# Kernel optimization log

Hardware: AMD Instinct MI355X
Metric: run time of the kernel (lower is better)

## Reference

```python
import jax, jax.numpy as jnp
from jax import lax
import numpy as np

DN = ('NCHW', 'OIHW', 'NCHW')

def conv2d(x, w, b, pad):
    y = lax.conv_general_dilated(x, w, (1, 1), [(pad, pad), (pad, pad)], dimension_numbers=DN)
    return y + b[None, :, None, None]

def setup_inputs() -> dict:
    key = jax.random.key(0)
    ks = jax.random.split(key, 20)
    B, C, H, W = 2, 256, 64, 64
    d = {}
    d['Fl'] = jax.random.normal(ks[0], (B, C, H, W), dtype=jnp.float32)
    d['Fv'] = jax.random.normal(ks[1], (B, C, H, W), dtype=jnp.float32)
    s3 = 1.0 / np.sqrt(C * 9)
    s1 = 1.0 / np.sqrt(C)
    names3 = ['Wqs', 'Wks', 'Wvs', 'Wqc', 'Wkc', 'Wvc']
    for i, n in enumerate(names3):
        d[n] = jax.random.normal(ks[2 + 2 * i], (C, C, 3, 3), dtype=jnp.float32) * s3
        d['b' + n[1:]] = jax.random.normal(ks[3 + 2 * i], (C,), dtype=jnp.float32) * 0.01
    d['Wgs'] = jax.random.normal(ks[14], (C, C, 1, 1), dtype=jnp.float32) * s1
    d['bgs'] = jax.random.normal(ks[15], (C,), dtype=jnp.float32) * 0.01
    d['Wfuse'] = jax.random.normal(ks[16], (C, 2 * C, 1, 1), dtype=jnp.float32) * (1.0 / np.sqrt(2 * C))
    d['bfuse'] = jax.random.normal(ks[17], (C,), dtype=jnp.float32) * 0.01
    return d

def reference(Fl, Fv, Wqs, bqs, Wks, bks, Wvs, bvs, Wqc, bqc, Wkc, bkc, Wvc, bvc, Wgs, bgs, Wfuse, bfuse):
    b, c, h, w = Fl.shape
    hw = h * w
    # --- self branch (on Fl) ---
    Qs = conv2d(Fl, Wqs, bqs, 1).reshape(b, c, hw)
    Ks = conv2d(Fl, Wks, bks, 1).reshape(b, c, hw)
    Vs = conv2d(Fl, Wvs, bvs, 1).reshape(b, c, hw)
    multi_s = jnp.einsum('bjk,bjq->bkq', Qs, Ks)          # [b, hw, hw]
    multi_s = jax.nn.softmax(multi_s, axis=1)              # softmax over dim=1 (as in torch code)
    Gs = jnp.einsum('bik,bjk->bij', multi_s, Vs)           # [b, hw, c]
    Gs = Gs.reshape(b, c, h, w)                            # raw reshape, faithful to torch
    Gs = conv2d(Gs, Wgs, bgs, 0) + Fl
    # --- cross branch (Q from Fl, K/V from Fv) ---
    Qc = conv2d(Fl, Wqc, bqc, 1).reshape(b, c, hw)
    Kc = conv2d(Fv, Wkc, bkc, 1).reshape(b, c, hw)
    Vc = conv2d(Fv, Wvc, bvc, 1).reshape(b, c, hw)
    multi_c = jnp.einsum('bjk,bjq->bkq', Qc, Kc)
    multi_c = jax.nn.softmax(multi_c, axis=1)
    Gc = jnp.einsum('bik,bjk->bij', multi_c, Vc)
    Gc = Gc.reshape(b, c, h, w)
    Gc = conv2d(Gc, Wgs, bgs, 0) + Fv                      # note: original uses Gs_conv for both branches
    out = conv2d(jnp.concatenate([Gs, Gc], axis=1), Wfuse, bfuse, 0)
    return out
```

## Files before the change

### kernel.cpp

```cpp
#include <hip/hip_runtime.h>

typedef __bf16 bf16x4 __attribute__((ext_vector_type(4)));
typedef __bf16 bf16x8 __attribute__((ext_vector_type(8)));
typedef float  f32x4  __attribute__((ext_vector_type(4)));

#define HWSZ 4096
#define CCH  256
#define LOG2E 1.44269504088896340736f

__device__ __forceinline__ float exp2_fast(float x) {
#if __has_builtin(__builtin_amdgcn_exp2f)
  return __builtin_amdgcn_exp2f(x);
#else
  return exp2f(x);
#endif
}

__device__ __forceinline__ void stage16(const __bf16* g, __bf16* ldsBase) {
#if __has_builtin(__builtin_amdgcn_global_load_lds)
  __builtin_amdgcn_global_load_lds(
      (const __attribute__((address_space(1))) void*)g,
      (__attribute__((address_space(3))) void*)ldsBase, 16, 0, 0);
#else
  int lane = threadIdx.x & 63;
  *(bf16x8*)(ldsBase + lane * 8) = *(const bf16x8*)g;
#endif
}

#define SWZ_STAGE(lane) ((((lane) & 3) ^ (((lane) >> 3) & 3)) * 8)
#define SWZ_READ(quad, lane) ((((quad) ^ (((lane) >> 1) & 3))) * 8)

__global__ __launch_bounds__(256)
void gemm_conv(const __bf16* __restrict__ AL, const __bf16* __restrict__ AV,
               const __bf16* __restrict__ Cc,
               __bf16* __restrict__ qst, __bf16* __restrict__ kst,
               __bf16* __restrict__ vs,  __bf16* __restrict__ qct,
               __bf16* __restrict__ kct, __bf16* __restrict__ vc,
               const float* __restrict__ bqs, const float* __restrict__ bks,
               const float* __restrict__ bvs, const float* __restrict__ bqc,
               const float* __restrict__ bkc, const float* __restrict__ bvc)
{
  __shared__ __align__(16) __bf16 smem[8192];
  __bf16* As = smem;
  __bf16* Bs = smem + 4096;

  const int tid  = threadIdx.x;
  const int lane = tid & 63;
  const int w    = tid >> 6;
  const int wm   = (w >> 1) * 64;
  const int wn   = (w & 1) * 64;
  const int z    = blockIdx.z;
  const int by   = blockIdx.y;
  const int bn   = blockIdx.x * 128;
  const int K    = 2304;

  const bool isL = (by < 8);
  const int bm = (isL ? by : by - 8) * 128;
  const __bf16* Ab = isL ? AL : AV;
  const __bf16* Bb = Cc + (long)((isL ? 0 : 2) + z) * 9437184;

  f32x4 acc[4][4] = {};
  const int srow = lane >> 2;
  const int skc  = SWZ_STAGE(lane);
  const int quad = lane >> 4, l15 = lane & 15;
  const int rdo  = SWZ_READ(quad, lane);

  for (int k0 = 0; k0 < K; k0 += 32) {
#pragma unroll
    for (int j = 0; j < 2; ++j) {
      int rbase = w * 32 + j * 16;
      stage16(Ab + (long)(bm + rbase + srow) * K + k0 + skc, As + rbase * 32);
    }
#pragma unroll
    for (int j = 0; j < 2; ++j) {
      int rbase = w * 32 + j * 16;
      stage16(Bb + (long)(bn + rbase + srow) * K + k0 + skc, Bs + rbase * 32);
    }
    __syncthreads();
    bf16x8 af[4], bfr[4];
#pragma unroll
    for (int t = 0; t < 4; ++t)
      af[t] = *(const bf16x8*)(As + (wm + t * 16 + l15) * 32 + rdo);
#pragma unroll
    for (int t = 0; t < 4; ++t)
      bfr[t] = *(const bf16x8*)(Bs + (wn + t * 16 + l15) * 32 + rdo);
#pragma unroll
    for (int mt = 0; mt < 4; ++mt)
#pragma unroll
      for (int nt = 0; nt < 4; ++nt)
        acc[mt][nt] = __builtin_amdgcn_mfma_f32_16x16x32_bf16(af[mt], bfr[nt], acc[mt][nt], 0, 0, 0);
    __syncthreads();
  }

#pragma unroll
  for (int mt = 0; mt < 4; ++mt) {
#pragma unroll
    for (int nt = 0; nt < 4; ++nt) {
#pragma unroll
      for (int r = 0; r < 4; ++r) {
        int m = bm + wm + mt * 16 + quad * 4 + r;
        int n = bn + wn + nt * 16 + l15;
        int g = m >> 8, mm = m & 255;
        const float* bias; __bf16* op; bool vlay;
        if (isL) {
          bias = (g == 0) ? bqs : (g == 1) ? bks : (g == 2) ? bvs : bqc;
          op   = (g == 0) ? qst : (g == 1) ? kst : (g == 2) ? vs  : qct;
          vlay = (g == 2);
        } else {
          bias = g ? bvc : bkc;
          op   = g ? vc  : kct;
          vlay = (g == 1);
        }
        float vv = acc[mt][nt][r] + bias[mm];
        if (vlay) op[(long)z * 1048576 + (long)mm * HWSZ + n] = (__bf16)vv;
        else      op[(long)z * 1048576 + (long)n * CCH + mm] = (__bf16)vv;
      }
    }
  }
}

__global__ __launch_bounds__(256)
void qk_stats(const __bf16* __restrict__ qs, const __bf16* __restrict__ qc,
              const __bf16* __restrict__ ks, const __bf16* __restrict__ kc,
              float* __restrict__ pm, float* __restrict__ pl)
{
  __shared__ __align__(16) __bf16 Kres[64 * 260];
  __shared__ float wm_[4][64], wl_[4][64];

  const int tid = threadIdx.x, lane = tid & 63, w = tid >> 6;
  const int quad = lane >> 4, l15 = lane & 15;
  const int lid = blockIdx.x;
  const int g = lid & 3;
  const int z = g & 1, br = g >> 1;
  const int ih = (lid >> 2) & 1;
  const int qb = (lid >> 3) * 64;
  const __bf16* Qt = (br ? qc : qs) + (long)z * 1048576;
  const __bf16* Kt = (br ? kc : ks) + (long)z * 1048576;

  for (int idx = tid; idx < 2048; idx += 256) {
    int r = idx >> 5, c8 = (idx & 31) * 8;
    *(bf16x8*)(Kres + r * 260 + c8) = *(const bf16x8*)(Kt + (long)(qb + r) * 256 + c8);
  }
  __syncthreads();

  float rm[4], rl[4];
#pragma unroll
  for (int nt = 0; nt < 4; ++nt) { rm[nt] = -3.0e38f; rl[nt] = 0.f; }

  for (int it = 0; it < 8; ++it) {
    const int i0 = ih * 2048 + it * 256 + w * 64;
    f32x4 accS[4][4] = {};
#pragma unroll
    for (int cs = 0; cs < 256; cs += 32) {
      bf16x8 a[4], b[4];
#pragma unroll
      for (int mt = 0; mt < 4; ++mt)
        a[mt] = *(const bf16x8*)(Qt + (long)(i0 + mt * 16 + l15) * 256 + cs + quad * 8);
#pragma unroll
      for (int nt = 0; nt < 4; ++nt)
        b[nt] = *(const bf16x8*)(Kres + (nt * 16 + l15) * 260 + cs + quad * 8);
#pragma unroll
      for (int mt = 0; mt < 4; ++mt)
#pragma unroll
        for (int nt = 0; nt < 4; ++nt)
          accS[mt][nt] = __builtin_amdgcn_mfma_f32_16x16x32_bf16(a[mt], b[nt], accS[mt][nt], 0, 0, 0);
    }
#pragma unroll
    for (int nt = 0; nt < 4; ++nt) {
      float mx = -3.0e38f;
#pragma unroll
      for (int mt = 0; mt < 4; ++mt)
#pragma unroll
        for (int r = 0; r < 4; ++r) mx = fmaxf(mx, accS[mt][nt][r]);
      float sl = 0.f;
#pragma unroll
      for (int mt = 0; mt < 4; ++mt)
#pragma unroll
        for (int r = 0; r < 4; ++r) sl += exp2_fast((accS[mt][nt][r] - mx) * LOG2E);
#pragma unroll
      for (int d = 16; d <= 32; d <<= 1) {
        float om = __shfl_xor(mx, d, 64);
        float ol = __shfl_xor(sl, d, 64);
        float nm = fmaxf(mx, om);
        sl = sl * exp2_fast((mx - nm) * LOG2E) + ol * exp2_fast((om - nm) * LOG2E);
        mx = nm;
      }
      float nm = fmaxf(rm[nt], mx);
      rl[nt] = rl[nt] * exp2_fast((rm[nt] - nm) * LOG2E) + sl * exp2_fast((mx - nm) * LOG2E);
      rm[nt] = nm;
    }
  }
  if (lane < 16) {
#pragma unroll
    for (int nt = 0; nt < 4; ++nt) { wm_[w][nt * 16 + lane] = rm[nt]; wl_[w][nt * 16 + lane] = rl[nt]; }
  }
  __syncthreads();
  if (tid < 64) {
    float m = -3.0e38f;
#pragma unroll
    for (int ww = 0; ww < 4; ++ww) m = fmaxf(m, wm_[ww][tid]);
    float l = 0.f;
#pragma unroll
    for (int ww = 0; ww < 4; ++ww)
      l += wl_[ww][tid] * exp2_fast((wm_[ww][tid] - m) * LOG2E);
    long o = ((long)ih * 4 + br * 2 + z) * 4096 + qb + tid;
    pm[o] = m;
    pl[o] = l;
  }
}

__global__ void stats_combine2(const float* __restrict__ pm, const float* __restrict__ pl,
                               float* __restrict__ mst, float* __restrict__ lst) {
  int q = blockIdx.x * 256 + threadIdx.x;
  int zbr = blockIdx.y;
  float m0 = pm[(long)zbr * 4096 + q],        l0 = pl[(long)zbr * 4096 + q];
  float m1 = pm[(long)(4 + zbr) * 4096 + q],  l1 = pl[(long)(4 + zbr) * 4096 + q];
  float m = fmaxf(m0, m1);
  float l = l0 * exp2_fast((m0 - m) * LOG2E) + l1 * exp2_fast((m1 - m) * LOG2E);
  mst[(long)zbr * 4096 + q] = m;
  lst[(long)zbr * 4096 + q] = 1.0f / l;
}

__global__ __launch_bounds__(256)
void fused_pv(const __bf16* __restrict__ qs, const __bf16* __restrict__ qc,
              const __bf16* __restrict__ ks, const __bf16* __restrict__ kc,
              const __bf16* __restrict__ vs, const __bf16* __restrict__ vc,
              const float* __restrict__ mst, const float* __restrict__ lst,
              float* __restrict__ gacc)
{
  __shared__ __align__(16) __bf16 Qres[64 * 260];
  __shared__ __align__(16) __bf16 Pl[64 * 132];
  __shared__ __align__(16) __bf16 Kst[128 * 32];

  const int tid = threadIdx.x, lane = tid & 63, w = tid >> 6;
  const int quad = lane >> 4, l15 = lane & 15;
  const int lid = blockIdx.x;
  const int g   = lid & 7;
  const int zbr = g >> 1;
  const int qh  = g & 1;
  const int bi  = (lid >> 3) * 64;
  const int br = zbr >> 1, z = zbr & 1;
  const __bf16* Qt = (br ? qc : qs) + (long)z * 1048576;
  const __bf16* Kt = (br ? kc : ks) + (long)z * 1048576;
  const __bf16* Vv = (br ? vc : vs) + (long)z * 1048576;
  const float* msp = mst + (long)zbr * 4096;
  const float* lsp = lst + (long)zbr * 4096;
  float* go = gacc + ((long)qh * 4 + zbr) * 1048576;

  for (int idx = tid; idx < 2048; idx += 256) {
    int r = idx >> 5, c8 = (idx & 31) * 8;
    *(bf16x8*)(Qres + r * 260 + c8) = *(const bf16x8*)(Qt + (long)(bi + r) * 256 + c8);
  }

  f32x4 accO[4][4] = {};
  const int srow = lane >> 2;
  const int skc  = SWZ_STAGE(lane);
  const int rdo  = SWZ_READ(quad, lane);
  const int q0 = qh * 2048;

  for (int qc0 = q0; qc0 < q0 + 2048; qc0 += 128) {
    f32x4 accS[4][2] = {};
#pragma unroll
    for (int cs = 0; cs < 256; cs += 32) {
#pragma unroll
      for (int jj = 0; jj < 2; ++jj) {
        int rbase = w * 32 + jj * 16;
        stage16(Kt + (long)(qc0 + rbase + srow) * 256 + cs + skc, Kst + rbase * 32);
      }
      __syncthreads();
      bf16x8 aq[4], bk[2];
#pragma unroll
      for (int mt = 0; mt < 4; ++mt)
        aq[mt] = *(const bf16x8*)(Qres + (mt * 16 + l15) * 260 + cs + quad * 8);
#pragma unroll
      for (int nt = 0; nt < 2; ++nt)
        bk[nt] = *(const bf16x8*)(Kst + (w * 32 + nt * 16 + l15) * 32 + rdo);
#pragma unroll
      for (int mt = 0; mt < 4; ++mt)
#pragma unroll
        for (int nt = 0; nt < 2; ++nt)
          accS[mt][nt] = __builtin_amdgcn_mfma_f32_16x16x32_bf16(aq[mt], bk[nt], accS[mt][nt], 0, 0, 0);
      __syncthreads();
    }
#pragma unroll
    for (int nt = 0; nt < 2; ++nt) {
      int q = w * 32 + nt * 16 + l15;
      float mq = msp[qc0 + q], lq = lsp[qc0 + q];
#pragma unroll
      for (int mt = 0; mt < 4; ++mt)
#pragma unroll
        for (int r = 0; r < 4; ++r) {
          int i = mt * 16 + quad * 4 + r;
          Pl[i * 132 + q] = (__bf16)(exp2_fast((accS[mt][nt][r] - mq) * LOG2E) * lq);
        }
    }
    __syncthreads();
#pragma unroll
    for (int qs0 = 0; qs0 < 128; qs0 += 32) {
      bf16x8 ap[4], bv[4];
#pragma unroll
      for (int mt = 0; mt < 4; ++mt)
        ap[mt] = *(const bf16x8*)(Pl + (mt * 16 + l15) * 132 + qs0 + quad * 8);
#pragma unroll
      for (int nt = 0; nt < 4; ++nt)
        bv[nt] = *(const bf16x8*)(Vv + (long)(w * 64 + nt * 16 + l15) * 4096 + qc0 + qs0 + quad * 8);
#pragma unroll
      for (int mt = 0; mt < 4; ++mt)
#pragma unroll
        for (int nt = 0; nt < 4; ++nt)
          accO[mt][nt] = __builtin_amdgcn_mfma_f32_16x16x32_bf16(ap[mt], bv[nt], accO[mt][nt], 0, 0, 0);
    }
  }
#pragma unroll
  for (int mt = 0; mt < 4; ++mt)
#pragma unroll
    for (int nt = 0; nt < 4; ++nt)
#pragma unroll
      for (int r = 0; r < 4; ++r) {
        int i = mt * 16 + quad * 4 + r;
        int j = w * 64 + nt * 16 + l15;
        go[(long)(bi + i) * 256 + j] = accO[mt][nt][r];
      }
}

__global__ __launch_bounds__(256)
void gsum_reshape(const float* __restrict__ ga, __bf16* __restrict__ gt) {
  __shared__ __bf16 lds[64 * 260];
  const int t = threadIdx.x, lane = t & 63, w = t >> 6;
  const int zbr = blockIdx.z;
  const int v   = blockIdx.y;
  const int jg  = blockIdx.x;
  const float* g0 = ga + (long)zbr * 1048576;
  const float* g1 = g0 + 4194304;
  for (int ci0 = 0; ci0 < 256; ci0 += 4) {
    int ci = ci0 + w;
    long src = (long)(ci * 16 + v) * 256 + jg * 64 + lane;
    lds[lane * 260 + ci] = (__bf16)(g0[src] + g1[src]);
  }
  __syncthreads();
  __bf16* out = gt + (long)zbr * 1048576 + ((long)v * 256 + jg * 64) * 256;
#pragma unroll
  for (int pp = 0; pp < 8; ++pp) {
    int idx = pp * 256 + t;
    int row = idx >> 5, c8 = (idx & 31) * 8;
    *(bf16x8*)(out + (long)row * 256 + c8) = *(const bf16x8*)(lds + row * 260 + c8);
  }
}

__global__ __launch_bounds__(256)
void wcomb(const float* __restrict__ Wgs, const float* __restrict__ bgs,
           const float* __restrict__ Wfu, const float* __restrict__ bfu,
           __bf16* __restrict__ WT, float* __restrict__ biasT)
{
  const int co = blockIdx.x, t = threadIdx.x;
  const float* wrow = Wfu + (long)co * 512;
  float accs = 0.f, accc = 0.f;
  for (int c = 0; c < 256; ++c) {
    float gv = Wgs[(long)c * 256 + t];
    accs = fmaf(wrow[c], gv, accs);
    accc = fmaf(wrow[c + 256], gv, accc);
  }
  __bf16* o = WT + (long)co * 1024;
  o[t]       = (__bf16)accs;
  o[256 + t] = (__bf16)accc;
  o[512 + t] = (__bf16)wrow[t];
  o[768 + t] = (__bf16)wrow[256 + t];
  __shared__ float red[256];
  red[t] = (wrow[t] + wrow[t + 256]) * bgs[t];
  __syncthreads();
  for (int s = 128; s > 0; s >>= 1) {
    if (t < s) red[t] += red[t + s];
    __syncthreads();
  }
  if (t == 0) biasT[co] = bfu[co] + red[0];
}

__global__ __launch_bounds__(256)
void tail_gemm(const __bf16* __restrict__ WT, const __bf16* __restrict__ GTS,
               const __bf16* __restrict__ Xt, const float* __restrict__ biasT,
               float* __restrict__ out)
{
  __shared__ __align__(16) __bf16 smem[8192];
  __bf16* As = smem;
  __bf16* Bs = smem + 4096;

  const int tid  = threadIdx.x;
  const int lane = tid & 63;
  const int w    = tid >> 6;
  const int wm   = (w >> 1) * 64;
  const int wn   = (w & 1) * 64;
  const int z    = blockIdx.z;
  const int bm   = blockIdx.y * 128;
  const int bn   = blockIdx.x * 128;

  const __bf16* Bsel[4] = {
    GTS + (long)z * 1048576, GTS + (long)(2 + z) * 1048576,
    Xt  + (long)z * 1048576, Xt  + (long)(2 + z) * 1048576
  };

  f32x4 acc[4][4] = {};
  const int srow = lane >> 2;
  const int skc  = SWZ_STAGE(lane);
  const int quad = lane >> 4, l15 = lane & 15;
  const int rdo  = SWZ_READ(quad, lane);

  for (int k0 = 0; k0 < 1024; k0 += 32) {
    const __bf16* Bb = Bsel[k0 >> 8];
    const int kk = k0 & 255;
#pragma unroll
    for (int j = 0; j < 2; ++j) {
      int rbase = w * 32 + j * 16;
      stage16(WT + (long)(bm + rbase + srow) * 1024 + k0 + skc, As + rbase * 32);
    }
#pragma unroll
    for (int j = 0; j < 2; ++j) {
      int rbase = w * 32 + j * 16;
      stage16(Bb + (long)(bn + rbase + srow) * 256 + kk + skc, Bs + rbase * 32);
    }
    __syncthreads();
    bf16x8 af[4], bfr[4];
#pragma unroll
    for (int t = 0; t < 4; ++t)
      af[t] = *(const bf16x8*)(As + (wm + t * 16 + l15) * 32 + rdo);
#pragma unroll
    for (int t = 0; t < 4; ++t)
      bfr[t] = *(const bf16x8*)(Bs + (wn + t * 16 + l15) * 32 + rdo);
#pragma unroll
    for (int mt = 0; mt < 4; ++mt)
#pragma unroll
      for (int nt = 0; nt < 4; ++nt)
        acc[mt][nt] = __builtin_amdgcn_mfma_f32_16x16x32_bf16(af[mt], bfr[nt], acc[mt][nt], 0, 0, 0);
    __syncthreads();
  }

#pragma unroll
  for (int mt = 0; mt < 4; ++mt)
#pragma unroll
    for (int nt = 0; nt < 4; ++nt)
#pragma unroll
      for (int r = 0; r < 4; ++r) {
        int m = bm + wm + mt * 16 + quad * 4 + r;
        int n = bn + wn + nt * 16 + l15;
        out[((long)z * 256 + m) * HWSZ + n] = acc[mt][nt][r] + biasT[m];
      }
}

__global__ void transpose_cvt(const float* __restrict__ F0, const float* __restrict__ F1,
                              __bf16* __restrict__ Xt) {
  __shared__ float tile[32][33];
  int img = blockIdx.z;
  const float* src = (img < 2 ? F0 : F1) + (long)(img & 1) * (CCH * HWSZ);
  __bf16* dst = Xt + (long)img * (HWSZ * CCH);
  int p0 = blockIdx.x * 32, c0 = blockIdx.y * 32;
  int tx = threadIdx.x, ty = threadIdx.y;
#pragma unroll
  for (int j = 0; j < 32; j += 8)
    tile[ty + j][tx] = src[(long)(c0 + ty + j) * HWSZ + p0 + tx];
  __syncthreads();
#pragma unroll
  for (int j = 0; j < 32; j += 8)
    dst[(long)(p0 + ty + j) * CCH + c0 + tx] = (__bf16)tile[tx][ty + j];
}

__global__ void im2col_k(const __bf16* __restrict__ Xt, __bf16* __restrict__ Cc) {
  int img = blockIdx.y;
  int e = blockIdx.x * 256 + threadIdx.x;
  int p = e / 288;
  int c8 = e - p * 288;
  int t = c8 >> 5;
  int ci0 = (c8 & 31) * 8;
  int dy = t / 3 - 1, dx = t - (t / 3) * 3 - 1;
  int y = p >> 6, x = p & 63;
  int yy = y + dy, xx = x + dx;
  const __bf16* src = Xt + (long)img * (HWSZ * CCH);
  __bf16* dst = Cc + (long)img * 9437184 + (long)p * 2304 + t * 256 + ci0;
  uint4 v = make_uint4(0u, 0u, 0u, 0u);
  if ((unsigned)yy < 64u && (unsigned)xx < 64u)
    v = *(const uint4*)(src + (long)(yy * 64 + xx) * CCH + ci0);
  *(uint4*)dst = v;
}

struct W6 { const float* w[6]; };
__global__ void repack_w3(W6 wp, __bf16* __restrict__ AL, __bf16* __restrict__ AV) {
  int zi = blockIdx.y;
  int e = blockIdx.x * 256 + threadIdx.x;
  int co = e / 2304;
  int rem = e - co * 2304;
  int t = rem >> 8, ci = rem & 255;
  float v = wp.w[zi][(long)co * 2304 + ci * 9 + t];
  __bf16* dst = (zi < 4) ? (AL + (long)zi * 256 * 2304) : (AV + (long)(zi - 4) * 256 * 2304);
  dst[(long)co * 2304 + rem] = (__bf16)v;
}

extern "C" void kernel_launch(void* const* d_in, const int* in_sizes, int n_in,
                              void* d_out, int out_size, void* d_ws, size_t ws_size,
                              hipStream_t stream) {
  const float* Fl  = (const float*)d_in[0];
  const float* Fv  = (const float*)d_in[1];
  const float* Wqs = (const float*)d_in[2];  const float* bqs = (const float*)d_in[3];
  const float* Wks = (const float*)d_in[4];  const float* bks = (const float*)d_in[5];
  const float* Wvs = (const float*)d_in[6];  const float* bvs = (const float*)d_in[7];
  const float* Wqc = (const float*)d_in[8];  const float* bqc = (const float*)d_in[9];
  const float* Wkc = (const float*)d_in[10]; const float* bkc = (const float*)d_in[11];
  const float* Wvc = (const float*)d_in[12]; const float* bvc = (const float*)d_in[13];
  const float* Wgs = (const float*)d_in[14]; const float* bgs = (const float*)d_in[15];
  const float* Wfu = (const float*)d_in[16]; const float* bfu = (const float*)d_in[17];

  char* ws = (char*)d_ws;
  size_t off = 0;
  auto take = [&](size_t bytes) -> void* {
    void* p = ws + off; off = (off + bytes + 255) & ~(size_t)255; return p;
  };
  __bf16* QST  = (__bf16*)take(4194304);
  __bf16* KST  = (__bf16*)take(4194304);
  __bf16* QCT  = (__bf16*)take(4194304);
  __bf16* KCT  = (__bf16*)take(4194304);
  __bf16* VS   = (__bf16*)take(4194304);
  __bf16* VC   = (__bf16*)take(4194304);
  __bf16* GTS  = (__bf16*)take(8388608);
  __bf16* AL   = (__bf16*)take(4718592);
  __bf16* AV   = (__bf16*)take(2359296);
  __bf16* WT   = (__bf16*)take(524288);
  float*  BT   = (float*)take(1024);
  float*  MST  = (float*)take(65536);
  float*  LST  = (float*)take(65536);
  float*  PM   = (float*)take(131072);
  float*  PL   = (float*)take(131072);
  __bf16* Xt   = (__bf16*)take(8388608);
  size_t ovl = off;
  __bf16* Cc = (__bf16*)take(75497472);
  size_t needConv = off;
  float* GACC = (float*)(ws + ovl);
  size_t needAttn = ovl + 33554432;
  size_t need = needConv > needAttn ? needConv : needAttn;
  if (ws_size < need) return;

  transpose_cvt<<<dim3(128, 8, 4), dim3(32, 8), 0, stream>>>(Fl, Fv, Xt);
  im2col_k<<<dim3(4608, 4), 256, 0, stream>>>(Xt, Cc);
  W6 wp; wp.w[0]=Wqs; wp.w[1]=Wks; wp.w[2]=Wvs; wp.w[3]=Wqc; wp.w[4]=Wkc; wp.w[5]=Wvc;
  repack_w3<<<dim3(2304, 6), 256, 0, stream>>>(wp, AL, AV);
  wcomb<<<dim3(256), 256, 0, stream>>>(Wgs, bgs, Wfu, bfu, WT, BT);

  gemm_conv<<<dim3(32, 12, 2), 256, 0, stream>>>(
      AL, AV, Cc, QST, KST, VS, QCT, KCT, VC,
      bqs, bks, bvs, bqc, bkc, bvc);

  qk_stats<<<dim3(512), 256, 0, stream>>>(QST, QCT, KST, KCT, PM, PL);
  stats_combine2<<<dim3(16, 4), 256, 0, stream>>>(PM, PL, MST, LST);

  fused_pv<<<dim3(512), 256, 0, stream>>>(
      QST, QCT, KST, KCT, VS, VC, MST, LST, GACC);

  gsum_reshape<<<dim3(4, 16, 4), 256, 0, stream>>>(GACC, GTS);

  tail_gemm<<<dim3(32, 2, 2), 256, 0, stream>>>(WT, GTS, Xt, BT, (float*)d_out);
}
```

Before: 442.9 us.

## Use 8 waves per block in fused_pv and read K directly from global

Doubles fused_pv's block size to 512 threads, so each wave computes a 16-column slice of the score tile and a 32-channel slice of the output, halving per-wave accumulator registers. The LDS staging of K tiles via global_load_lds, and its two barriers per k-step, is dropped; each wave now loads its K fragment straight from global memory. The aim is higher occupancy and fewer barriers, at the cost of uncoalesced, uncached-in-LDS K reads and more waves contending on the same Qres/Pl tiles.

```diff
diff --git a/kernel.cpp b/kernel.cpp
--- a/kernel.cpp
+++ b/kernel.cpp
@@ -221,7 +221,7 @@
   lst[(long)zbr * 4096 + q] = 1.0f / l;
 }
 
-__global__ __launch_bounds__(256)
+__global__ __launch_bounds__(512, 4)
 void fused_pv(const __bf16* __restrict__ qs, const __bf16* __restrict__ qc,
               const __bf16* __restrict__ ks, const __bf16* __restrict__ kc,
               const __bf16* __restrict__ vs, const __bf16* __restrict__ vc,
@@ -230,7 +230,6 @@
 {
   __shared__ __align__(16) __bf16 Qres[64 * 260];
   __shared__ __align__(16) __bf16 Pl[64 * 132];
-  __shared__ __align__(16) __bf16 Kst[128 * 32];
 
   const int tid = threadIdx.x, lane = tid & 63, w = tid >> 6;
   const int quad = lane >> 4, l15 = lane & 15;
@@ -247,78 +246,67 @@
   const float* lsp = lst + (long)zbr * 4096;
   float* go = gacc + ((long)qh * 4 + zbr) * 1048576;
 
-  for (int idx = tid; idx < 2048; idx += 256) {
+  for (int idx = tid; idx < 2048; idx += 512) {
     int r = idx >> 5, c8 = (idx & 31) * 8;
     *(bf16x8*)(Qres + r * 260 + c8) = *(const bf16x8*)(Qt + (long)(bi + r) * 256 + c8);
   }
-
-  f32x4 accO[4][4] = {};
-  const int srow = lane >> 2;
-  const int skc  = SWZ_STAGE(lane);
-  const int rdo  = SWZ_READ(quad, lane);
+  __syncthreads();
+
+  f32x4 accO[4][2] = {};
   const int q0 = qh * 2048;
+  const __bf16* Vl0 = Vv + (long)(w * 32 + l15) * 4096 + quad * 8;
+  const __bf16* Vl1 = Vl0 + (long)16 * 4096;
 
   for (int qc0 = q0; qc0 < q0 + 2048; qc0 += 128) {
-    f32x4 accS[4][2] = {};
+    f32x4 accS[4] = {};
+    const __bf16* Kl = Kt + (long)(qc0 + w * 16 + l15) * 256 + quad * 8;
 #pragma unroll
     for (int cs = 0; cs < 256; cs += 32) {
-#pragma unroll
-      for (int jj = 0; jj < 2; ++jj) {
-        int rbase = w * 32 + jj * 16;
-        stage16(Kt + (long)(qc0 + rbase + srow) * 256 + cs + skc, Kst + rbase * 32);
-      }
-      __syncthreads();
-      bf16x8 aq[4], bk[2];
+      bf16x8 aq[4];
+      bf16x8 bk = *(const bf16x8*)(Kl + cs);
 #pragma unroll
       for (int mt = 0; mt < 4; ++mt)
         aq[mt] = *(const bf16x8*)(Qres + (mt * 16 + l15) * 260 + cs + quad * 8);
 #pragma unroll
-      for (int nt = 0; nt < 2; ++nt)
-        bk[nt] = *(const bf16x8*)(Kst + (w * 32 + nt * 16 + l15) * 32 + rdo);
-#pragma unroll
-      for (int mt = 0; mt < 4; ++mt)
-#pragma unroll
-        for (int nt = 0; nt < 2; ++nt)
-          accS[mt][nt] = __builtin_amdgcn_mfma_f32_16x16x32_bf16(aq[mt], bk[nt], accS[mt][nt], 0, 0, 0);
-      __syncthreads();
-    }
-#pragma unroll
-    for (int nt = 0; nt < 2; ++nt) {
-      int q = w * 32 + nt * 16 + l15;
+      for (int mt = 0; mt < 4; ++mt)
+        accS[mt] = __builtin_amdgcn_mfma_f32_16x16x32_bf16(aq[mt], bk, accS[mt], 0, 0, 0);
+    }
+    __syncthreads();
+    {
+      int q = w * 16 + l15;
       float mq = msp[qc0 + q], lq = lsp[qc0 + q];
 #pragma unroll
       for (int mt = 0; mt < 4; ++mt)
 #pragma unroll
         for (int r = 0; r < 4; ++r) {
           int i = mt * 16 + quad * 4 + r;
-          Pl[i * 132 + q] = (__bf16)(exp2_fast((accS[mt][nt][r] - mq) * LOG2E) * lq);
+          Pl[i * 132 + q] = (__bf16)(exp2_fast((accS[mt][r] - mq) * LOG2E) * lq);
         }
     }
     __syncthreads();
 #pragma unroll
     for (int qs0 = 0; qs0 < 128; qs0 += 32) {
-      bf16x8 ap[4], bv[4];
+      bf16x8 ap[4], bv0, bv1;
+      bv0 = *(const bf16x8*)(Vl0 + qc0 + qs0);
+      bv1 = *(const bf16x8*)(Vl1 + qc0 + qs0);
 #pragma unroll
       for (int mt = 0; mt < 4; ++mt)
         ap[mt] = *(const bf16x8*)(Pl + (mt * 16 + l15) * 132 + qs0 + quad * 8);
 #pragma unroll
-      for (int nt = 0; nt < 4; ++nt)
-        bv[nt] = *(const bf16x8*)(Vv + (long)(w * 64 + nt * 16 + l15) * 4096 + qc0 + qs0 + quad * 8);
-#pragma unroll
-      for (int mt = 0; mt < 4; ++mt)
-#pragma unroll
-        for (int nt = 0; nt < 4; ++nt)
-          accO[mt][nt] = __builtin_amdgcn_mfma_f32_16x16x32_bf16(ap[mt], bv[nt], accO[mt][nt], 0, 0, 0);
+      for (int mt = 0; mt < 4; ++mt) {
+        accO[mt][0] = __builtin_amdgcn_mfma_f32_16x16x32_bf16(ap[mt], bv0, accO[mt][0], 0, 0, 0);
+        accO[mt][1] = __builtin_amdgcn_mfma_f32_16x16x32_bf16(ap[mt], bv1, accO[mt][1], 0, 0, 0);
+      }
     }
   }
 #pragma unroll
   for (int mt = 0; mt < 4; ++mt)
 #pragma unroll
-    for (int nt = 0; nt < 4; ++nt)
+    for (int nt = 0; nt < 2; ++nt)
 #pragma unroll
       for (int r = 0; r < 4; ++r) {
         int i = mt * 16 + quad * 4 + r;
-        int j = w * 64 + nt * 16 + l15;
+        int j = w * 32 + nt * 16 + l15;
         go[(long)(bi + i) * 256 + j] = accO[mt][nt][r];
       }
 }
@@ -548,7 +536,7 @@
   qk_stats<<<dim3(512), 256, 0, stream>>>(QST, QCT, KST, KCT, PM, PL);
   stats_combine2<<<dim3(16, 4), 256, 0, stream>>>(PM, PL, MST, LST);
 
-  fused_pv<<<dim3(512), 256, 0, stream>>>(
+  fused_pv<<<dim3(512), 512, 0, stream>>>(
       QST, QCT, KST, KCT, VS, VC, MST, LST, GACC);
 
   gsum_reshape<<<dim3(4, 16, 4), 256, 0, stream>>>(GACC, GTS);
```

Result: slower. 455.4 us (+2.8%).

## Unfuse attention into materialized P matrix plus split-K PV GEMM per branch

Applied to the files above, without the earlier changes.

Replaces the fused QK-softmax-PV kernel with three per-branch kernels. The first writes the normalized bf16 probability matrix (4096x4096) to global memory, the second runs a split-K GEMM of P against V into four partial buffers, and the third sums the partials and reshapes. The aim is to avoid recomputing or serialising the QK and PV phases inside one kernel and to give the PV product a cleaner GEMM tiling. In exchange it writes and re-reads a 32MB P matrix per branch and launches twelve kernels instead of two.

```diff
diff --git a/kernel.cpp b/kernel.cpp
--- a/kernel.cpp
+++ b/kernel.cpp
@@ -1,6 +1,5 @@
 #include <hip/hip_runtime.h>
 
-typedef __bf16 bf16x4 __attribute__((ext_vector_type(4)));
 typedef __bf16 bf16x8 __attribute__((ext_vector_type(8)));
 typedef float  f32x4  __attribute__((ext_vector_type(4)));
 
@@ -222,120 +221,138 @@
 }
 
 __global__ __launch_bounds__(256)
-void fused_pv(const __bf16* __restrict__ qs, const __bf16* __restrict__ qc,
-              const __bf16* __restrict__ ks, const __bf16* __restrict__ kc,
-              const __bf16* __restrict__ vs, const __bf16* __restrict__ vc,
-              const float* __restrict__ mst, const float* __restrict__ lst,
-              float* __restrict__ gacc)
+void pmat(const __bf16* __restrict__ qs, const __bf16* __restrict__ qc,
+          const __bf16* __restrict__ ks, const __bf16* __restrict__ kc,
+          const float* __restrict__ mst, const float* __restrict__ lst,
+          __bf16* __restrict__ Pg, int zbr)
 {
-  __shared__ __align__(16) __bf16 Qres[64 * 260];
-  __shared__ __align__(16) __bf16 Pl[64 * 132];
-  __shared__ __align__(16) __bf16 Kst[128 * 32];
-
+  __shared__ __align__(16) __bf16 Kres[64 * 260];
   const int tid = threadIdx.x, lane = tid & 63, w = tid >> 6;
   const int quad = lane >> 4, l15 = lane & 15;
   const int lid = blockIdx.x;
-  const int g   = lid & 7;
-  const int zbr = g >> 1;
-  const int qh  = g & 1;
-  const int bi  = (lid >> 3) * 64;
+  const int ihq = lid & 7;
+  const int qb = (lid >> 3) * 64;
   const int br = zbr >> 1, z = zbr & 1;
   const __bf16* Qt = (br ? qc : qs) + (long)z * 1048576;
   const __bf16* Kt = (br ? kc : ks) + (long)z * 1048576;
-  const __bf16* Vv = (br ? vc : vs) + (long)z * 1048576;
   const float* msp = mst + (long)zbr * 4096;
   const float* lsp = lst + (long)zbr * 4096;
-  float* go = gacc + ((long)qh * 4 + zbr) * 1048576;
 
   for (int idx = tid; idx < 2048; idx += 256) {
     int r = idx >> 5, c8 = (idx & 31) * 8;
-    *(bf16x8*)(Qres + r * 260 + c8) = *(const bf16x8*)(Qt + (long)(bi + r) * 256 + c8);
-  }
-
-  f32x4 accO[4][4] = {};
+    *(bf16x8*)(Kres + r * 260 + c8) = *(const bf16x8*)(Kt + (long)(qb + r) * 256 + c8);
+  }
+  __syncthreads();
+
+  float mq[4], lq[4];
+#pragma unroll
+  for (int nt = 0; nt < 4; ++nt) {
+    int q = qb + nt * 16 + l15;
+    mq[nt] = msp[q];
+    lq[nt] = lsp[q];
+  }
+
+  for (int it = 0; it < 2; ++it) {
+    const int i0 = ihq * 512 + it * 256 + w * 64;
+    f32x4 accS[4][4] = {};
+#pragma unroll
+    for (int cs = 0; cs < 256; cs += 32) {
+      bf16x8 a[4], b[4];
+#pragma unroll
+      for (int mt = 0; mt < 4; ++mt)
+        a[mt] = *(const bf16x8*)(Qt + (long)(i0 + mt * 16 + l15) * 256 + cs + quad * 8);
+#pragma unroll
+      for (int nt = 0; nt < 4; ++nt)
+        b[nt] = *(const bf16x8*)(Kres + (nt * 16 + l15) * 260 + cs + quad * 8);
+#pragma unroll
+      for (int mt = 0; mt < 4; ++mt)
+#pragma unroll
+        for (int nt = 0; nt < 4; ++nt)
+          accS[mt][nt] = __builtin_amdgcn_mfma_f32_16x16x32_bf16(a[mt], b[nt], accS[mt][nt], 0, 0, 0);
+    }
+#pragma unroll
+    for (int nt = 0; nt < 4; ++nt) {
+      const int q = qb + nt * 16 + l15;
+#pragma unroll
+      for (int mt = 0; mt < 4; ++mt)
+#pragma unroll
+        for (int r = 0; r < 4; ++r) {
+          int i = i0 + mt * 16 + quad * 4 + r;
+          Pg[(long)i * 4096 + q] =
+              (__bf16)(exp2_fast((accS[mt][nt][r] - mq[nt]) * LOG2E) * lq[nt]);
+        }
+    }
+  }
+}
+
+__global__ __launch_bounds__(256)
+void pv_gemm(const __bf16* __restrict__ Pg, const __bf16* __restrict__ vs,
+             const __bf16* __restrict__ vc, float* __restrict__ gpart, int zbr)
+{
+  __shared__ __align__(16) __bf16 smem[10240];
+  __bf16* As = smem;
+  __bf16* Bs = smem + 2048;
+
+  const int tid = threadIdx.x, lane = tid & 63, w = tid >> 6;
+  const int quad = lane >> 4, l15 = lane & 15;
   const int srow = lane >> 2;
   const int skc  = SWZ_STAGE(lane);
   const int rdo  = SWZ_READ(quad, lane);
-  const int q0 = qh * 2048;
-
-  for (int qc0 = q0; qc0 < q0 + 2048; qc0 += 128) {
-    f32x4 accS[4][2] = {};
-#pragma unroll
-    for (int cs = 0; cs < 256; cs += 32) {
-#pragma unroll
-      for (int jj = 0; jj < 2; ++jj) {
-        int rbase = w * 32 + jj * 16;
-        stage16(Kt + (long)(qc0 + rbase + srow) * 256 + cs + skc, Kst + rbase * 32);
+  const int kq = blockIdx.x;
+  const int bm = blockIdx.y * 64;
+  const int br = zbr >> 1, z = zbr & 1;
+  const __bf16* Vv = (br ? vc : vs) + (long)z * 1048576;
+  const int wn = w * 64;
+
+  f32x4 acc[4][4] = {};
+
+  for (int k0 = kq * 1024; k0 < kq * 1024 + 1024; k0 += 32) {
+    stage16(Pg + (long)(bm + w * 16 + srow) * 4096 + k0 + skc, As + (w * 16) * 32);
+#pragma unroll
+    for (int jj = 0; jj < 4; ++jj) {
+      int rb = wn + jj * 16;
+      stage16(Vv + (long)(rb + srow) * 4096 + k0 + skc, Bs + rb * 32);
+    }
+    __syncthreads();
+    bf16x8 af[4], bfr[4];
+#pragma unroll
+    for (int t = 0; t < 4; ++t)
+      af[t] = *(const bf16x8*)(As + (t * 16 + l15) * 32 + rdo);
+#pragma unroll
+    for (int t = 0; t < 4; ++t)
+      bfr[t] = *(const bf16x8*)(Bs + (wn + t * 16 + l15) * 32 + rdo);
+#pragma unroll
+    for (int mt = 0; mt < 4; ++mt)
+#pragma unroll
+      for (int nt = 0; nt < 4; ++nt)
+        acc[mt][nt] = __builtin_amdgcn_mfma_f32_16x16x32_bf16(af[mt], bfr[nt], acc[mt][nt], 0, 0, 0);
+    __syncthreads();
+  }
+
+  float* go = gpart + (long)kq * 1048576;
+#pragma unroll
+  for (int mt = 0; mt < 4; ++mt)
+#pragma unroll
+    for (int nt = 0; nt < 4; ++nt)
+#pragma unroll
+      for (int r = 0; r < 4; ++r) {
+        int i = bm + mt * 16 + quad * 4 + r;
+        int j = wn + nt * 16 + l15;
+        go[(long)i * 256 + j] = acc[mt][nt][r];
       }
-      __syncthreads();
-      bf16x8 aq[4], bk[2];
-#pragma unroll
-      for (int mt = 0; mt < 4; ++mt)
-        aq[mt] = *(const bf16x8*)(Qres + (mt * 16 + l15) * 260 + cs + quad * 8);
-#pragma unroll
-      for (int nt = 0; nt < 2; ++nt)
-        bk[nt] = *(const bf16x8*)(Kst + (w * 32 + nt * 16 + l15) * 32 + rdo);
-#pragma unroll
-      for (int mt = 0; mt < 4; ++mt)
-#pragma unroll
-        for (int nt = 0; nt < 2; ++nt)
-          accS[mt][nt] = __builtin_amdgcn_mfma_f32_16x16x32_bf16(aq[mt], bk[nt], accS[mt][nt], 0, 0, 0);
-      __syncthreads();
-    }
-#pragma unroll
-    for (int nt = 0; nt < 2; ++nt) {
-      int q = w * 32 + nt * 16 + l15;
-      float mq = msp[qc0 + q], lq = lsp[qc0 + q];
-#pragma unroll
-      for (int mt = 0; mt < 4; ++mt)
-#pragma unroll
-        for (int r = 0; r < 4; ++r) {
-          int i = mt * 16 + quad * 4 + r;
-          Pl[i * 132 + q] = (__bf16)(exp2_fast((accS[mt][nt][r] - mq) * LOG2E) * lq);
-        }
-    }
-    __syncthreads();
-#pragma unroll
-    for (int qs0 = 0; qs0 < 128; qs0 += 32) {
-      bf16x8 ap[4], bv[4];
-#pragma unroll
-      for (int mt = 0; mt < 4; ++mt)
-        ap[mt] = *(const bf16x8*)(Pl + (mt * 16 + l15) * 132 + qs0 + quad * 8);
-#pragma unroll
-      for (int nt = 0; nt < 4; ++nt)
-        bv[nt] = *(const bf16x8*)(Vv + (long)(w * 64 + nt * 16 + l15) * 4096 + qc0 + qs0 + quad * 8);
-#pragma unroll
-      for (int mt = 0; mt < 4; ++mt)
-#pragma unroll
-        for (int nt = 0; nt < 4; ++nt)
-          accO[mt][nt] = __builtin_amdgcn_mfma_f32_16x16x32_bf16(ap[mt], bv[nt], accO[mt][nt], 0, 0, 0);
-    }
-  }
-#pragma unroll
-  for (int mt = 0; mt < 4; ++mt)
-#pragma unroll
-    for (int nt = 0; nt < 4; ++nt)
-#pragma unroll
-      for (int r = 0; r < 4; ++r) {
-        int i = mt * 16 + quad * 4 + r;
-        int j = w * 64 + nt * 16 + l15;
-        go[(long)(bi + i) * 256 + j] = accO[mt][nt][r];
-      }
-}
-
-__global__ __launch_bounds__(256)
-void gsum_reshape(const float* __restrict__ ga, __bf16* __restrict__ gt) {
+}
+
+__global__ __launch_bounds__(256)
+void gsum_reshape(const float* __restrict__ ga, __bf16* __restrict__ gt, int zbr) {
   __shared__ __bf16 lds[64 * 260];
   const int t = threadIdx.x, lane = t & 63, w = t >> 6;
-  const int zbr = blockIdx.z;
   const int v   = blockIdx.y;
   const int jg  = blockIdx.x;
-  const float* g0 = ga + (long)zbr * 1048576;
-  const float* g1 = g0 + 4194304;
   for (int ci0 = 0; ci0 < 256; ci0 += 4) {
     int ci = ci0 + w;
     long src = (long)(ci * 16 + v) * 256 + jg * 64 + lane;
-    lds[lane * 260 + ci] = (__bf16)(g0[src] + g1[src]);
+    float s = ga[src] + ga[src + 1048576] + ga[src + 2097152] + ga[src + 3145728];
+    lds[lane * 260 + ci] = (__bf16)s;
   }
   __syncthreads();
   __bf16* out = gt + (long)zbr * 1048576 + ((long)v * 256 + jg * 64) * 256;
@@ -530,8 +547,9 @@
   size_t ovl = off;
   __bf16* Cc = (__bf16*)take(75497472);
   size_t needConv = off;
-  float* GACC = (float*)(ws + ovl);
-  size_t needAttn = ovl + 33554432;
+  __bf16* Pg  = (__bf16*)(ws + ovl);
+  float*  GIJ = (float*)(ws + ovl + 33554432);
+  size_t needAttn = ovl + 33554432 + 16777216;
   size_t need = needConv > needAttn ? needConv : needAttn;
   if (ws_size < need) return;
 
@@ -548,10 +566,11 @@
   qk_stats<<<dim3(512), 256, 0, stream>>>(QST, QCT, KST, KCT, PM, PL);
   stats_combine2<<<dim3(16, 4), 256, 0, stream>>>(PM, PL, MST, LST);
 
-  fused_pv<<<dim3(512), 256, 0, stream>>>(
-      QST, QCT, KST, KCT, VS, VC, MST, LST, GACC);
-
-  gsum_reshape<<<dim3(4, 16, 4), 256, 0, stream>>>(GACC, GTS);
+  for (int zbr = 0; zbr < 4; ++zbr) {
+    pmat<<<dim3(512), 256, 0, stream>>>(QST, QCT, KST, KCT, MST, LST, Pg, zbr);
+    pv_gemm<<<dim3(4, 64), 256, 0, stream>>>(Pg, VS, VC, GIJ, zbr);
+    gsum_reshape<<<dim3(4, 16), 256, 0, stream>>>(GIJ, GTS, zbr);
+  }
 
   tail_gemm<<<dim3(32, 2, 2), 256, 0, stream>>>(WT, GTS, Xt, BT, (float*)d_out);
 }
```

New measurement: 584.1 us. 31.9% more time.
